# Kernel tuning notes

Measured on AMD Instinct MI355X. Metric: run time of the kernel, lower is better.

## Reference

```python
import jax, jax.numpy as jnp
import numpy as np

N = 10000
E = 320000
IN_DIM = 1
HD = 32
OUT_DIM = 1


def _lin(k, fan_in, fan_out):
    k1, k2 = jax.random.split(k)
    bound = 1.0 / np.sqrt(fan_in)
    W = jax.random.uniform(k1, (fan_in, fan_out), minval=-bound, maxval=bound, dtype=jnp.float32)
    b = jax.random.uniform(k2, (fan_out,), minval=-bound, maxval=bound, dtype=jnp.float32)
    return W, b


def setup_inputs() -> dict:
    key = jax.random.key(0)
    ks = jax.random.split(key, 12)
    sources = jax.random.randint(ks[0], (E,), 0, N)
    dests = jax.random.randint(ks[1], (E,), 0, N)
    weights = jax.random.uniform(ks[2], (E, 1), dtype=jnp.float32)
    x = jax.random.normal(ks[3], (N, IN_DIM), dtype=jnp.float32)
    h = jax.random.normal(ks[4], (N, HD), dtype=jnp.float32)
    W_enc, b_enc = _lin(ks[5], IN_DIM + HD, HD)
    W_msg, b_msg = _lin(ks[6], 2 * HD + 1, HD)
    W_upd, b_upd = _lin(ks[7], 2 * HD, HD)
    W_dec, b_dec = _lin(ks[8], 2 * HD, OUT_DIM)
    W_term, b_term = _lin(ks[9], HD, 1)
    W_pred, b_pred = _lin(ks[10], 2 * HD + 1, 1)
    return {"sources": sources, "dests": dests, "weights": weights, "x": x, "h": h,
            "W_enc": W_enc, "b_enc": b_enc, "W_msg": W_msg, "b_msg": b_msg,
            "W_upd": W_upd, "b_upd": b_upd, "W_dec": W_dec, "b_dec": b_dec,
            "W_term": W_term, "b_term": b_term, "W_pred": W_pred, "b_pred": b_pred}


def reference(sources, dests, weights, x, h, W_enc, b_enc, W_msg, b_msg,
              W_upd, b_upd, W_dec, b_dec, W_term, b_term, W_pred, b_pred):
    n = h.shape[0]
    # Encoder: z = Linear(cat[x, h])
    z = jnp.concatenate([x, h], axis=1) @ W_enc + b_enc  # [N, HD]
    # Processor messages: Linear(cat[z[dest], z[src], w])
    msg_in = jnp.concatenate([z[dests], z[sources], weights], axis=1)  # [E, 2*HD+1]
    messages = msg_in @ W_msg + b_msg  # [E, HD]
    # scatter-amax into destination nodes, -inf (no edge) -> 0
    m = jnp.full((n, HD), -jnp.inf, dtype=z.dtype).at[dests].max(messages)
    m = jnp.where(jnp.isneginf(m), jnp.zeros_like(m), m)
    h_new = jnp.concatenate([z, m], axis=1) @ W_upd + b_upd  # [N, HD]
    # Decoder
    y = jnp.concatenate([z, h_new], axis=1) @ W_dec + b_dec  # [N, 1]
    # Termination: proj of mean node state -> scalar
    t = (h_new.mean(axis=0) @ W_term + b_term).squeeze()
    # Predecessor: dense N x N score matrix, edge entries set to proj score
    pred_in = jnp.concatenate([h_new[dests], h_new[sources], weights], axis=1)
    edge_scores = (pred_in @ W_pred + b_pred)[:, 0]  # [E]
    p = jnp.full((n, n), -1e9, dtype=h_new.dtype).at[dests, sources].set(edge_scores)
    return (y, p, h_new, t)
```

## Files before the change

kernel.cpp:

```cpp
#include <hip/hip_runtime.h>
#include <stdint.h>

namespace {
constexpr int  kN  = 10000;
constexpr int  kE  = 320000;
constexpr long kPOff = 10000;
constexpr long kHOff = 10000L + 100000000L;
constexpr long kTOff = kHOff + 320000L;
constexpr long kP4   = (long)kN * kN / 4;
constexpr long kFillA = kP4 * 15 / 100;
constexpr long kFillB = kP4 * 80 / 100;
constexpr int  kG = 2048;
}

typedef float f32x4 __attribute__((ext_vector_type(4)));

__device__ __forceinline__ float shfl32(float v, int k) { return __shfl(v, k, 32); }

__device__ __forceinline__ void fill_slice(float* __restrict__ p, long lo, long hi)
{
    long idx = (long)blockIdx.x * blockDim.x + threadIdx.x;
    long stride = (long)gridDim.x * blockDim.x;
    f32x4 v = { -1e9f, -1e9f, -1e9f, -1e9f };
    f32x4* p4 = reinterpret_cast<f32x4*>(p);
    for (long i = lo + idx; i < hi; i += stride)
        p4[i] = v;
}

__global__ __launch_bounds__(256) void k1_encz(
    const float* __restrict__ x, const float* __restrict__ h,
    const float* __restrict__ W_enc, const float* __restrict__ b_enc,
    const float* __restrict__ W_msg, const float* __restrict__ b_msg,
    float* __restrict__ z, float* __restrict__ zwd, float* __restrict__ zws,
    float* __restrict__ m, float* __restrict__ sum_h, float* __restrict__ p)
{
    if (blockIdx.x == 0 && threadIdx.x < 32) sum_h[threadIdx.x] = 0.0f;

    int lane = threadIdx.x & 63;
    int wid  = threadIdx.x >> 6;
    int half = lane >> 5;
    int j    = lane & 31;

    for (int i = blockIdx.x * 8 + wid * 2 + half; i < kN; i += kG * 8) {
        float hj = h[(long)i * 32 + j];
        float xi = x[i];
        float zj = fmaf(xi, W_enc[j], b_enc[j]);
#pragma unroll
        for (int k = 0; k < 32; ++k)
            zj = fmaf(shfl32(hj, k), W_enc[(1 + k) * 32 + j], zj);

        z[(long)i * 32 + j] = zj;
        m[(long)i * 32 + j] = -__builtin_inff();

        float dv = b_msg[j], sv = 0.0f;
#pragma unroll
        for (int k = 0; k < 32; ++k) {
            float zk = shfl32(zj, k);
            dv = fmaf(zk, W_msg[k * 32 + j], dv);
            sv = fmaf(zk, W_msg[(32 + k) * 32 + j], sv);
        }
        zwd[(long)i * 32 + j] = dv;
        zws[(long)i * 32 + j] = sv;
    }

    fill_slice(p, 0, kFillA);
}

__global__ __launch_bounds__(256) void k2_msgmax(
    const int* __restrict__ src, const int* __restrict__ dst,
    const float* __restrict__ w, const float* __restrict__ zwd,
    const float* __restrict__ zws, const float* __restrict__ W_msg,
    float* __restrict__ m, float* __restrict__ p)
{
    int lane = threadIdx.x & 63;
    int wid  = threadIdx.x >> 6;
    int half = lane >> 5;
    int j    = lane & 31;
    float Ww = W_msg[64 * 32 + j];
    int gw = blockIdx.x * 4 + wid;
    for (int ep = gw; ep < kE / 2; ep += kG * 4) {
        int e = ep * 2 + half;
        int d = dst[e], s = src[e];
        float val = fmaf(w[e], Ww, zwd[(long)d * 32 + j] + zws[(long)s * 32 + j]);
        float* addr = m + (long)d * 32 + j;
        if (val >= 0.0f)
            atomicMax(reinterpret_cast<int*>(addr), __float_as_int(val));
        else
            atomicMin(reinterpret_cast<unsigned int*>(addr), __float_as_uint(val));
    }

    fill_slice(p, kFillA, kFillB);
}

__global__ __launch_bounds__(256) void k3_updn(
    const float* __restrict__ z, const float* __restrict__ m,
    const float* __restrict__ W_upd, const float* __restrict__ b_upd,
    const float* __restrict__ W_dec, const float* __restrict__ b_dec,
    const float* __restrict__ W_pred,
    float* __restrict__ y_out, float* __restrict__ h_out,
    float* __restrict__ a_out, float* __restrict__ b_out,
    float* __restrict__ sum_h, float* __restrict__ p)
{
    int i = blockIdx.x * 256 + threadIdx.x;
    if (i < ((kN + 255) & ~255)) {
        bool valid = i < kN;
        int ii = valid ? i : (kN - 1);

        float acc[32];
#pragma unroll
        for (int jj = 0; jj < 32; ++jj) acc[jj] = b_upd[jj];
        float yv = b_dec[0];

        const float4* z4 = reinterpret_cast<const float4*>(z + (long)ii * 32);
#pragma unroll
        for (int q = 0; q < 8; ++q) {
            float4 v = z4[q];
            float in0 = v.x, in1 = v.y, in2 = v.z, in3 = v.w;
            int k = q * 4;
            yv = fmaf(in0, W_dec[k + 0], yv);
            yv = fmaf(in1, W_dec[k + 1], yv);
            yv = fmaf(in2, W_dec[k + 2], yv);
            yv = fmaf(in3, W_dec[k + 3], yv);
            const float* W0 = W_upd + (k + 0) * 32;
            const float* W1 = W_upd + (k + 1) * 32;
            const float* W2 = W_upd + (k + 2) * 32;
            const float* W3 = W_upd + (k + 3) * 32;
#pragma unroll
            for (int jj = 0; jj < 32; ++jj) acc[jj] = fmaf(in0, W0[jj], acc[jj]);
#pragma unroll
            for (int jj = 0; jj < 32; ++jj) acc[jj] = fmaf(in1, W1[jj], acc[jj]);
#pragma unroll
            for (int jj = 0; jj < 32; ++jj) acc[jj] = fmaf(in2, W2[jj], acc[jj]);
#pragma unroll
            for (int jj = 0; jj < 32; ++jj) acc[jj] = fmaf(in3, W3[jj], acc[jj]);
        }

        const float NEG_INF = -__builtin_inff();
        const float4* m4 = reinterpret_cast<const float4*>(m + (long)ii * 32);
#pragma unroll
        for (int q = 0; q < 8; ++q) {
            float4 v = m4[q];
            float in0 = (v.x == NEG_INF) ? 0.0f : v.x;
            float in1 = (v.y == NEG_INF) ? 0.0f : v.y;
            float in2 = (v.z == NEG_INF) ? 0.0f : v.z;
            float in3 = (v.w == NEG_INF) ? 0.0f : v.w;
            int k = 32 + q * 4;
            const float* W0 = W_upd + (k + 0) * 32;
            const float* W1 = W_upd + (k + 1) * 32;
            const float* W2 = W_upd + (k + 2) * 32;
            const float* W3 = W_upd + (k + 3) * 32;
#pragma unroll
            for (int jj = 0; jj < 32; ++jj) acc[jj] = fmaf(in0, W0[jj], acc[jj]);
#pragma unroll
            for (int jj = 0; jj < 32; ++jj) acc[jj] = fmaf(in1, W1[jj], acc[jj]);
#pragma unroll
            for (int jj = 0; jj < 32; ++jj) acc[jj] = fmaf(in2, W2[jj], acc[jj]);
#pragma unroll
            for (int jj = 0; jj < 32; ++jj) acc[jj] = fmaf(in3, W3[jj], acc[jj]);
        }

        float av = 0.0f, bv = 0.0f;
#pragma unroll
        for (int k = 0; k < 32; ++k) {
            yv = fmaf(acc[k], W_dec[32 + k], yv);
            av = fmaf(acc[k], W_pred[k], av);
            bv = fmaf(acc[k], W_pred[32 + k], bv);
        }

        if (valid) {
            y_out[i] = yv;
            a_out[i] = av;
            b_out[i] = bv;
            float4* hrow = reinterpret_cast<float4*>(h_out + (long)i * 32);
#pragma unroll
            for (int q = 0; q < 8; ++q)
                hrow[q] = make_float4(acc[q * 4 + 0], acc[q * 4 + 1],
                                      acc[q * 4 + 2], acc[q * 4 + 3]);
        }

#pragma unroll
        for (int jj = 0; jj < 32; ++jj) {
            float v = valid ? acc[jj] : 0.0f;
#pragma unroll
            for (int off = 32; off; off >>= 1) v += __shfl_down(v, off, 64);
            if ((threadIdx.x & 63) == 0) atomicAdd(sum_h + jj, v);
        }
    }

    fill_slice(p, kFillB, kP4);
}

__global__ __launch_bounds__(256) void k4_pred(
    const int* __restrict__ src, const int* __restrict__ dst,
    const float* __restrict__ w, const float* __restrict__ a,
    const float* __restrict__ b, const float* __restrict__ W_pred,
    const float* __restrict__ b_pred, const float* __restrict__ sum_h,
    const float* __restrict__ W_term, const float* __restrict__ b_term,
    float* __restrict__ t_out, float* __restrict__ p)
{
    if (blockIdx.x == 0 && threadIdx.x < 64) {
        int l = threadIdx.x;
        float s = (l < 32) ? (sum_h[l] * (1.0f / (float)kN)) * W_term[l] : 0.0f;
#pragma unroll
        for (int off = 32; off; off >>= 1) s += __shfl_down(s, off, 64);
        if (l == 0) t_out[0] = s + b_term[0];
    }

    for (int e = blockIdx.x * 256 + threadIdx.x; e < kE; e += kG * 256) {
        int d = dst[e], s = src[e];
        float score = a[d] + b[s] + fmaf(w[e], W_pred[64], b_pred[0]);
        p[(long)d * kN + s] = score;
    }
}

extern "C" void kernel_launch(void* const* d_in, const int* in_sizes, int n_in,
                              void* d_out, int out_size, void* d_ws, size_t ws_size,
                              hipStream_t stream)
{
    const int*   sources = (const int*)d_in[0];
    const int*   dests   = (const int*)d_in[1];
    const float* weights = (const float*)d_in[2];
    const float* x       = (const float*)d_in[3];
    const float* h       = (const float*)d_in[4];
    const float* W_enc   = (const float*)d_in[5];
    const float* b_enc   = (const float*)d_in[6];
    const float* W_msg   = (const float*)d_in[7];
    const float* b_msg   = (const float*)d_in[8];
    const float* W_upd   = (const float*)d_in[9];
    const float* b_upd   = (const float*)d_in[10];
    const float* W_dec   = (const float*)d_in[11];
    const float* b_dec   = (const float*)d_in[12];
    const float* W_term  = (const float*)d_in[13];
    const float* b_term  = (const float*)d_in[14];
    const float* W_pred  = (const float*)d_in[15];
    const float* b_pred  = (const float*)d_in[16];

    float* out   = (float*)d_out;
    float* y_out = out;
    float* p_out = out + kPOff;
    float* h_out = out + kHOff;
    float* t_out = out + kTOff;

    float* z     = (float*)d_ws;
    float* m     = z   + (long)kN * 32;
    float* zwd   = m   + (long)kN * 32;
    float* zws   = zwd + (long)kN * 32;
    float* a_ws  = zws + (long)kN * 32;
    float* b_ws  = a_ws + kN;
    float* sum_h = b_ws + kN;

    k1_encz<<<kG, 256, 0, stream>>>(x, h, W_enc, b_enc, W_msg, b_msg,
                                    z, zwd, zws, m, sum_h, p_out);
    k2_msgmax<<<kG, 256, 0, stream>>>(sources, dests, weights, zwd, zws, W_msg,
                                      m, p_out);
    k3_updn<<<kG, 256, 0, stream>>>(z, m, W_upd, b_upd, W_dec, b_dec, W_pred,
                                    y_out, h_out, a_ws, b_ws, sum_h, p_out);
    k4_pred<<<kG, 256, 0, stream>>>(sources, dests, weights, a_ws, b_ws,
                                    W_pred, b_pred, sum_h, W_term, b_term,
                                    t_out, p_out);
}
```

Measured before the change: 599.1 us.

## Replicate max-aggregation buffer and move dense fill into a standalone kernel

The scatter-max target is replicated eight ways, with each block choosing a replica by block index. This spreads atomic contention, and the update kernel then reduces the replicas with fmax. The 400MB fill of the predecessor matrix is no longer split across the first three kernels; it now runs in its own kernel just before the edge-scatter kernel, and grid sizes are matched to each kernel's work. The cost is eight times more memory to initialise and to read back in the update step. Moving the fill out of the other kernels also removes any overlap it had with their compute.

```diff
diff --git a/kernel.cpp b/kernel.cpp
--- a/kernel.cpp
+++ b/kernel.cpp
@@ -4,193 +4,201 @@
 namespace {
 constexpr int  kN  = 10000;
 constexpr int  kE  = 320000;
+constexpr int  kR  = 8;
 constexpr long kPOff = 10000;
 constexpr long kHOff = 10000L + 100000000L;
 constexpr long kTOff = kHOff + 320000L;
-constexpr long kP4   = (long)kN * kN / 4;
-constexpr long kFillA = kP4 * 15 / 100;
-constexpr long kFillB = kP4 * 80 / 100;
-constexpr int  kG = 2048;
 }
 
 typedef float f32x4 __attribute__((ext_vector_type(4)));
 
 __device__ __forceinline__ float shfl32(float v, int k) { return __shfl(v, k, 32); }
-
-__device__ __forceinline__ void fill_slice(float* __restrict__ p, long lo, long hi)
-{
-    long idx = (long)blockIdx.x * blockDim.x + threadIdx.x;
-    long stride = (long)gridDim.x * blockDim.x;
-    f32x4 v = { -1e9f, -1e9f, -1e9f, -1e9f };
-    f32x4* p4 = reinterpret_cast<f32x4*>(p);
-    for (long i = lo + idx; i < hi; i += stride)
-        p4[i] = v;
-}
 
 __global__ __launch_bounds__(256) void k1_encz(
     const float* __restrict__ x, const float* __restrict__ h,
     const float* __restrict__ W_enc, const float* __restrict__ b_enc,
     const float* __restrict__ W_msg, const float* __restrict__ b_msg,
     float* __restrict__ z, float* __restrict__ zwd, float* __restrict__ zws,
-    float* __restrict__ m, float* __restrict__ sum_h, float* __restrict__ p)
+    float* __restrict__ m_rep, float* __restrict__ sum_h)
 {
     if (blockIdx.x == 0 && threadIdx.x < 32) sum_h[threadIdx.x] = 0.0f;
+
+    {
+        const float NEG_INF = -__builtin_inff();
+        f32x4 vinf = { NEG_INF, NEG_INF, NEG_INF, NEG_INF };
+        f32x4* r4 = reinterpret_cast<f32x4*>(m_rep);
+        long total4 = (long)kR * kN * 32 / 4;
+        long idx = (long)blockIdx.x * 256 + threadIdx.x;
+        long stride = (long)gridDim.x * 256;
+        for (long i = idx; i < total4; i += stride) r4[i] = vinf;
+    }
 
     int lane = threadIdx.x & 63;
     int wid  = threadIdx.x >> 6;
     int half = lane >> 5;
     int j    = lane & 31;
-
-    for (int i = blockIdx.x * 8 + wid * 2 + half; i < kN; i += kG * 8) {
-        float hj = h[(long)i * 32 + j];
-        float xi = x[i];
-        float zj = fmaf(xi, W_enc[j], b_enc[j]);
-#pragma unroll
-        for (int k = 0; k < 32; ++k)
-            zj = fmaf(shfl32(hj, k), W_enc[(1 + k) * 32 + j], zj);
-
-        z[(long)i * 32 + j] = zj;
-        m[(long)i * 32 + j] = -__builtin_inff();
-
-        float dv = b_msg[j], sv = 0.0f;
-#pragma unroll
-        for (int k = 0; k < 32; ++k) {
-            float zk = shfl32(zj, k);
-            dv = fmaf(zk, W_msg[k * 32 + j], dv);
-            sv = fmaf(zk, W_msg[(32 + k) * 32 + j], sv);
-        }
-        zwd[(long)i * 32 + j] = dv;
-        zws[(long)i * 32 + j] = sv;
-    }
-
-    fill_slice(p, 0, kFillA);
+    int i = blockIdx.x * 8 + wid * 2 + half;
+    if (i >= kN) return;
+
+    float hj = h[(long)i * 32 + j];
+    float xi = x[i];
+    float zj = fmaf(xi, W_enc[j], b_enc[j]);
+#pragma unroll
+    for (int k = 0; k < 32; ++k)
+        zj = fmaf(shfl32(hj, k), W_enc[(1 + k) * 32 + j], zj);
+
+    z[(long)i * 32 + j] = zj;
+
+    float dv = b_msg[j], sv = 0.0f;
+#pragma unroll
+    for (int k = 0; k < 32; ++k) {
+        float zk = shfl32(zj, k);
+        dv = fmaf(zk, W_msg[k * 32 + j], dv);
+        sv = fmaf(zk, W_msg[(32 + k) * 32 + j], sv);
+    }
+    zwd[(long)i * 32 + j] = dv;
+    zws[(long)i * 32 + j] = sv;
 }
 
 __global__ __launch_bounds__(256) void k2_msgmax(
     const int* __restrict__ src, const int* __restrict__ dst,
     const float* __restrict__ w, const float* __restrict__ zwd,
     const float* __restrict__ zws, const float* __restrict__ W_msg,
-    float* __restrict__ m, float* __restrict__ p)
+    float* __restrict__ m_rep)
 {
     int lane = threadIdx.x & 63;
     int wid  = threadIdx.x >> 6;
     int half = lane >> 5;
     int j    = lane & 31;
     float Ww = W_msg[64 * 32 + j];
+    float* mr = m_rep + (long)(blockIdx.x & (kR - 1)) * kN * 32;
+
     int gw = blockIdx.x * 4 + wid;
-    for (int ep = gw; ep < kE / 2; ep += kG * 4) {
+    int nw = gridDim.x * 4;
+    for (int ep = gw; ep < kE / 2; ep += nw) {
         int e = ep * 2 + half;
         int d = dst[e], s = src[e];
         float val = fmaf(w[e], Ww, zwd[(long)d * 32 + j] + zws[(long)s * 32 + j]);
-        float* addr = m + (long)d * 32 + j;
+        float* addr = mr + (long)d * 32 + j;
         if (val >= 0.0f)
             atomicMax(reinterpret_cast<int*>(addr), __float_as_int(val));
         else
             atomicMin(reinterpret_cast<unsigned int*>(addr), __float_as_uint(val));
     }
-
-    fill_slice(p, kFillA, kFillB);
 }
 
 __global__ __launch_bounds__(256) void k3_updn(
-    const float* __restrict__ z, const float* __restrict__ m,
+    const float* __restrict__ z, const float* __restrict__ m_rep,
     const float* __restrict__ W_upd, const float* __restrict__ b_upd,
     const float* __restrict__ W_dec, const float* __restrict__ b_dec,
     const float* __restrict__ W_pred,
     float* __restrict__ y_out, float* __restrict__ h_out,
     float* __restrict__ a_out, float* __restrict__ b_out,
-    float* __restrict__ sum_h, float* __restrict__ p)
+    float* __restrict__ sum_h)
 {
     int i = blockIdx.x * 256 + threadIdx.x;
-    if (i < ((kN + 255) & ~255)) {
-        bool valid = i < kN;
-        int ii = valid ? i : (kN - 1);
-
-        float acc[32];
-#pragma unroll
-        for (int jj = 0; jj < 32; ++jj) acc[jj] = b_upd[jj];
-        float yv = b_dec[0];
-
-        const float4* z4 = reinterpret_cast<const float4*>(z + (long)ii * 32);
-#pragma unroll
-        for (int q = 0; q < 8; ++q) {
-            float4 v = z4[q];
-            float in0 = v.x, in1 = v.y, in2 = v.z, in3 = v.w;
-            int k = q * 4;
-            yv = fmaf(in0, W_dec[k + 0], yv);
-            yv = fmaf(in1, W_dec[k + 1], yv);
-            yv = fmaf(in2, W_dec[k + 2], yv);
-            yv = fmaf(in3, W_dec[k + 3], yv);
-            const float* W0 = W_upd + (k + 0) * 32;
-            const float* W1 = W_upd + (k + 1) * 32;
-            const float* W2 = W_upd + (k + 2) * 32;
-            const float* W3 = W_upd + (k + 3) * 32;
-#pragma unroll
-            for (int jj = 0; jj < 32; ++jj) acc[jj] = fmaf(in0, W0[jj], acc[jj]);
-#pragma unroll
-            for (int jj = 0; jj < 32; ++jj) acc[jj] = fmaf(in1, W1[jj], acc[jj]);
-#pragma unroll
-            for (int jj = 0; jj < 32; ++jj) acc[jj] = fmaf(in2, W2[jj], acc[jj]);
-#pragma unroll
-            for (int jj = 0; jj < 32; ++jj) acc[jj] = fmaf(in3, W3[jj], acc[jj]);
+    bool valid = i < kN;
+    int ii = valid ? i : (kN - 1);
+
+    float acc[32];
+#pragma unroll
+    for (int jj = 0; jj < 32; ++jj) acc[jj] = b_upd[jj];
+    float yv = b_dec[0];
+
+    const float4* z4 = reinterpret_cast<const float4*>(z + (long)ii * 32);
+#pragma unroll
+    for (int q = 0; q < 8; ++q) {
+        float4 v = z4[q];
+        float in0 = v.x, in1 = v.y, in2 = v.z, in3 = v.w;
+        int k = q * 4;
+        yv = fmaf(in0, W_dec[k + 0], yv);
+        yv = fmaf(in1, W_dec[k + 1], yv);
+        yv = fmaf(in2, W_dec[k + 2], yv);
+        yv = fmaf(in3, W_dec[k + 3], yv);
+        const float* W0 = W_upd + (k + 0) * 32;
+        const float* W1 = W_upd + (k + 1) * 32;
+        const float* W2 = W_upd + (k + 2) * 32;
+        const float* W3 = W_upd + (k + 3) * 32;
+#pragma unroll
+        for (int jj = 0; jj < 32; ++jj) acc[jj] = fmaf(in0, W0[jj], acc[jj]);
+#pragma unroll
+        for (int jj = 0; jj < 32; ++jj) acc[jj] = fmaf(in1, W1[jj], acc[jj]);
+#pragma unroll
+        for (int jj = 0; jj < 32; ++jj) acc[jj] = fmaf(in2, W2[jj], acc[jj]);
+#pragma unroll
+        for (int jj = 0; jj < 32; ++jj) acc[jj] = fmaf(in3, W3[jj], acc[jj]);
+    }
+
+    const float NEG_INF = -__builtin_inff();
+#pragma unroll
+    for (int q = 0; q < 8; ++q) {
+        const float4* m4 = reinterpret_cast<const float4*>(m_rep + (long)ii * 32) + q;
+        float4 v = *m4;
+#pragma unroll
+        for (int r = 1; r < kR; ++r) {
+            float4 t = *(m4 + (long)r * kN * 8);
+            v.x = fmaxf(v.x, t.x); v.y = fmaxf(v.y, t.y);
+            v.z = fmaxf(v.z, t.z); v.w = fmaxf(v.w, t.w);
         }
-
-        const float NEG_INF = -__builtin_inff();
-        const float4* m4 = reinterpret_cast<const float4*>(m + (long)ii * 32);
-#pragma unroll
-        for (int q = 0; q < 8; ++q) {
-            float4 v = m4[q];
-            float in0 = (v.x == NEG_INF) ? 0.0f : v.x;
-            float in1 = (v.y == NEG_INF) ? 0.0f : v.y;
-            float in2 = (v.z == NEG_INF) ? 0.0f : v.z;
-            float in3 = (v.w == NEG_INF) ? 0.0f : v.w;
-            int k = 32 + q * 4;
-            const float* W0 = W_upd + (k + 0) * 32;
-            const float* W1 = W_upd + (k + 1) * 32;
-            const float* W2 = W_upd + (k + 2) * 32;
-            const float* W3 = W_upd + (k + 3) * 32;
-#pragma unroll
-            for (int jj = 0; jj < 32; ++jj) acc[jj] = fmaf(in0, W0[jj], acc[jj]);
-#pragma unroll
-            for (int jj = 0; jj < 32; ++jj) acc[jj] = fmaf(in1, W1[jj], acc[jj]);
-#pragma unroll
-            for (int jj = 0; jj < 32; ++jj) acc[jj] = fmaf(in2, W2[jj], acc[jj]);
-#pragma unroll
-            for (int jj = 0; jj < 32; ++jj) acc[jj] = fmaf(in3, W3[jj], acc[jj]);
-        }
-
-        float av = 0.0f, bv = 0.0f;
-#pragma unroll
-        for (int k = 0; k < 32; ++k) {
-            yv = fmaf(acc[k], W_dec[32 + k], yv);
-            av = fmaf(acc[k], W_pred[k], av);
-            bv = fmaf(acc[k], W_pred[32 + k], bv);
-        }
-
-        if (valid) {
-            y_out[i] = yv;
-            a_out[i] = av;
-            b_out[i] = bv;
-            float4* hrow = reinterpret_cast<float4*>(h_out + (long)i * 32);
-#pragma unroll
-            for (int q = 0; q < 8; ++q)
-                hrow[q] = make_float4(acc[q * 4 + 0], acc[q * 4 + 1],
-                                      acc[q * 4 + 2], acc[q * 4 + 3]);
-        }
-
-#pragma unroll
-        for (int jj = 0; jj < 32; ++jj) {
-            float v = valid ? acc[jj] : 0.0f;
-#pragma unroll
-            for (int off = 32; off; off >>= 1) v += __shfl_down(v, off, 64);
-            if ((threadIdx.x & 63) == 0) atomicAdd(sum_h + jj, v);
-        }
-    }
-
-    fill_slice(p, kFillB, kP4);
-}
-
-__global__ __launch_bounds__(256) void k4_pred(
+        float in0 = (v.x == NEG_INF) ? 0.0f : v.x;
+        float in1 = (v.y == NEG_INF) ? 0.0f : v.y;
+        float in2 = (v.z == NEG_INF) ? 0.0f : v.z;
+        float in3 = (v.w == NEG_INF) ? 0.0f : v.w;
+        int k = 32 + q * 4;
+        const float* W0 = W_upd + (k + 0) * 32;
+        const float* W1 = W_upd + (k + 1) * 32;
+        const float* W2 = W_upd + (k + 2) * 32;
+        const float* W3 = W_upd + (k + 3) * 32;
+#pragma unroll
+        for (int jj = 0; jj < 32; ++jj) acc[jj] = fmaf(in0, W0[jj], acc[jj]);
+#pragma unroll
+        for (int jj = 0; jj < 32; ++jj) acc[jj] = fmaf(in1, W1[jj], acc[jj]);
+#pragma unroll
+        for (int jj = 0; jj < 32; ++jj) acc[jj] = fmaf(in2, W2[jj], acc[jj]);
+#pragma unroll
+        for (int jj = 0; jj < 32; ++jj) acc[jj] = fmaf(in3, W3[jj], acc[jj]);
+    }
+
+    float av = 0.0f, bv = 0.0f;
+#pragma unroll
+    for (int k = 0; k < 32; ++k) {
+        yv = fmaf(acc[k], W_dec[32 + k], yv);
+        av = fmaf(acc[k], W_pred[k], av);
+        bv = fmaf(acc[k], W_pred[32 + k], bv);
+    }
+
+    if (valid) {
+        y_out[i] = yv;
+        a_out[i] = av;
+        b_out[i] = bv;
+        float4* hrow = reinterpret_cast<float4*>(h_out + (long)i * 32);
+#pragma unroll
+        for (int q = 0; q < 8; ++q)
+            hrow[q] = make_float4(acc[q * 4 + 0], acc[q * 4 + 1],
+                                  acc[q * 4 + 2], acc[q * 4 + 3]);
+    }
+
+#pragma unroll
+    for (int jj = 0; jj < 32; ++jj) {
+        float v = valid ? acc[jj] : 0.0f;
+#pragma unroll
+        for (int off = 32; off; off >>= 1) v += __shfl_down(v, off, 64);
+        if ((threadIdx.x & 63) == 0) atomicAdd(sum_h + jj, v);
+    }
+}
+
+__global__ __launch_bounds__(256) void k4_fill(float* __restrict__ p)
+{
+    long idx = (long)blockIdx.x * 256 + threadIdx.x;
+    long stride = (long)gridDim.x * 256;
+    const long total4 = (long)kN * (long)kN / 4;
+    f32x4 v = { -1e9f, -1e9f, -1e9f, -1e9f };
+    f32x4* p4 = reinterpret_cast<f32x4*>(p);
+    for (long i = idx; i < total4; i += stride)
+        p4[i] = v;
+}
+
+__global__ __launch_bounds__(256) void k5_pred(
     const int* __restrict__ src, const int* __restrict__ dst,
     const float* __restrict__ w, const float* __restrict__ a,
     const float* __restrict__ b, const float* __restrict__ W_pred,
@@ -206,11 +214,11 @@
         if (l == 0) t_out[0] = s + b_term[0];
     }
 
-    for (int e = blockIdx.x * 256 + threadIdx.x; e < kE; e += kG * 256) {
-        int d = dst[e], s = src[e];
-        float score = a[d] + b[s] + fmaf(w[e], W_pred[64], b_pred[0]);
-        p[(long)d * kN + s] = score;
-    }
+    int e = blockIdx.x * 256 + threadIdx.x;
+    if (e >= kE) return;
+    int d = dst[e], s = src[e];
+    float score = a[d] + b[s] + fmaf(w[e], W_pred[64], b_pred[0]);
+    p[(long)d * kN + s] = score;
 }
 
 extern "C" void kernel_launch(void* const* d_in, const int* in_sizes, int n_in,
@@ -242,20 +250,20 @@
     float* t_out = out + kTOff;
 
     float* z     = (float*)d_ws;
-    float* m     = z   + (long)kN * 32;
-    float* zwd   = m   + (long)kN * 32;
+    float* zwd   = z   + (long)kN * 32;
     float* zws   = zwd + (long)kN * 32;
     float* a_ws  = zws + (long)kN * 32;
     float* b_ws  = a_ws + kN;
     float* sum_h = b_ws + kN;
-
-    k1_encz<<<kG, 256, 0, stream>>>(x, h, W_enc, b_enc, W_msg, b_msg,
-                                    z, zwd, zws, m, sum_h, p_out);
-    k2_msgmax<<<kG, 256, 0, stream>>>(sources, dests, weights, zwd, zws, W_msg,
-                                      m, p_out);
-    k3_updn<<<kG, 256, 0, stream>>>(z, m, W_upd, b_upd, W_dec, b_dec, W_pred,
-                                    y_out, h_out, a_ws, b_ws, sum_h, p_out);
-    k4_pred<<<kG, 256, 0, stream>>>(sources, dests, weights, a_ws, b_ws,
-                                    W_pred, b_pred, sum_h, W_term, b_term,
-                                    t_out, p_out);
-}
+    float* m_rep = sum_h + 32;
+
+    k1_encz<<<(kN + 7) / 8, 256, 0, stream>>>(x, h, W_enc, b_enc, W_msg, b_msg,
+                                              z, zwd, zws, m_rep, sum_h);
+    k2_msgmax<<<2048, 256, 0, stream>>>(sources, dests, weights, zwd, zws, W_msg, m_rep);
+    k3_updn<<<(kN + 255) / 256, 256, 0, stream>>>(z, m_rep, W_upd, b_upd, W_dec, b_dec,
+                                                  W_pred, y_out, h_out, a_ws, b_ws, sum_h);
+    k4_fill<<<8192, 256, 0, stream>>>(p_out);
+    k5_pred<<<(kE + 255) / 256, 256, 0, stream>>>(sources, dests, weights, a_ws, b_ws,
+                                                  W_pred, b_pred, sum_h, W_term, b_term,
+                                                  t_out, p_out);
+}
```

Result: no change. 609.1 us (+1.7%).

## Consolidate dense P fill into message kernel via block specialization

Applied to the files above, without the earlier changes.

Moves the entire -1e9 fill of the N×N score matrix into the edge message/scatter-max kernel, dedicating odd blocks to the fill and even blocks to the atomic scatter. The encoder, update and predecessor kernels lose their fill slices and are launched with exact-size grids instead of grid-stride loops over 2048 blocks. The aim is to overlap the bandwidth-bound fill with the latency-bound atomic scatter and to make the other kernels short. In exchange, only half the blocks of one kernel drive the 400 MB fill, which may underuse memory bandwidth compared with spreading it across three kernels.

```diff
diff --git a/kernel.cpp b/kernel.cpp
--- a/kernel.cpp
+++ b/kernel.cpp
@@ -8,31 +8,18 @@
 constexpr long kHOff = 10000L + 100000000L;
 constexpr long kTOff = kHOff + 320000L;
 constexpr long kP4   = (long)kN * kN / 4;
-constexpr long kFillA = kP4 * 15 / 100;
-constexpr long kFillB = kP4 * 80 / 100;
-constexpr int  kG = 2048;
 }
 
 typedef float f32x4 __attribute__((ext_vector_type(4)));
 
 __device__ __forceinline__ float shfl32(float v, int k) { return __shfl(v, k, 32); }
-
-__device__ __forceinline__ void fill_slice(float* __restrict__ p, long lo, long hi)
-{
-    long idx = (long)blockIdx.x * blockDim.x + threadIdx.x;
-    long stride = (long)gridDim.x * blockDim.x;
-    f32x4 v = { -1e9f, -1e9f, -1e9f, -1e9f };
-    f32x4* p4 = reinterpret_cast<f32x4*>(p);
-    for (long i = lo + idx; i < hi; i += stride)
-        p4[i] = v;
-}
 
 __global__ __launch_bounds__(256) void k1_encz(
     const float* __restrict__ x, const float* __restrict__ h,
     const float* __restrict__ W_enc, const float* __restrict__ b_enc,
     const float* __restrict__ W_msg, const float* __restrict__ b_msg,
     float* __restrict__ z, float* __restrict__ zwd, float* __restrict__ zws,
-    float* __restrict__ m, float* __restrict__ sum_h, float* __restrict__ p)
+    float* __restrict__ m, float* __restrict__ sum_h)
 {
     if (blockIdx.x == 0 && threadIdx.x < 32) sum_h[threadIdx.x] = 0.0f;
 
@@ -40,56 +27,64 @@
     int wid  = threadIdx.x >> 6;
     int half = lane >> 5;
     int j    = lane & 31;
-
-    for (int i = blockIdx.x * 8 + wid * 2 + half; i < kN; i += kG * 8) {
-        float hj = h[(long)i * 32 + j];
-        float xi = x[i];
-        float zj = fmaf(xi, W_enc[j], b_enc[j]);
-#pragma unroll
-        for (int k = 0; k < 32; ++k)
-            zj = fmaf(shfl32(hj, k), W_enc[(1 + k) * 32 + j], zj);
-
-        z[(long)i * 32 + j] = zj;
-        m[(long)i * 32 + j] = -__builtin_inff();
-
-        float dv = b_msg[j], sv = 0.0f;
-#pragma unroll
-        for (int k = 0; k < 32; ++k) {
-            float zk = shfl32(zj, k);
-            dv = fmaf(zk, W_msg[k * 32 + j], dv);
-            sv = fmaf(zk, W_msg[(32 + k) * 32 + j], sv);
-        }
-        zwd[(long)i * 32 + j] = dv;
-        zws[(long)i * 32 + j] = sv;
-    }
-
-    fill_slice(p, 0, kFillA);
-}
-
-__global__ __launch_bounds__(256) void k2_msgmax(
+    int i = blockIdx.x * 8 + wid * 2 + half;
+    if (i >= kN) return;
+
+    float hj = h[(long)i * 32 + j];
+    float xi = x[i];
+    float zj = fmaf(xi, W_enc[j], b_enc[j]);
+#pragma unroll
+    for (int k = 0; k < 32; ++k)
+        zj = fmaf(shfl32(hj, k), W_enc[(1 + k) * 32 + j], zj);
+
+    z[(long)i * 32 + j] = zj;
+    m[(long)i * 32 + j] = -__builtin_inff();
+
+    float dv = b_msg[j], sv = 0.0f;
+#pragma unroll
+    for (int k = 0; k < 32; ++k) {
+        float zk = shfl32(zj, k);
+        dv = fmaf(zk, W_msg[k * 32 + j], dv);
+        sv = fmaf(zk, W_msg[(32 + k) * 32 + j], sv);
+    }
+    zwd[(long)i * 32 + j] = dv;
+    zws[(long)i * 32 + j] = sv;
+}
+
+__global__ __launch_bounds__(256) void k2_work(
     const int* __restrict__ src, const int* __restrict__ dst,
     const float* __restrict__ w, const float* __restrict__ zwd,
     const float* __restrict__ zws, const float* __restrict__ W_msg,
     float* __restrict__ m, float* __restrict__ p)
 {
-    int lane = threadIdx.x & 63;
-    int wid  = threadIdx.x >> 6;
-    int half = lane >> 5;
-    int j    = lane & 31;
-    float Ww = W_msg[64 * 32 + j];
-    int gw = blockIdx.x * 4 + wid;
-    for (int ep = gw; ep < kE / 2; ep += kG * 4) {
-        int e = ep * 2 + half;
-        int d = dst[e], s = src[e];
-        float val = fmaf(w[e], Ww, zwd[(long)d * 32 + j] + zws[(long)s * 32 + j]);
-        float* addr = m + (long)d * 32 + j;
-        if (val >= 0.0f)
-            atomicMax(reinterpret_cast<int*>(addr), __float_as_int(val));
-        else
-            atomicMin(reinterpret_cast<unsigned int*>(addr), __float_as_uint(val));
-    }
-
-    fill_slice(p, kFillA, kFillB);
+    if (blockIdx.x & 1) {
+        long fb = blockIdx.x >> 1;
+        long idx = fb * 256 + threadIdx.x;
+        long stride = 1024L * 256;
+        f32x4 v = { -1e9f, -1e9f, -1e9f, -1e9f };
+        f32x4* p4 = reinterpret_cast<f32x4*>(p);
+        for (long i = idx; i < kP4; i += stride)
+            p4[i] = v;
+    } else {
+        int lane = threadIdx.x & 63;
+        int wid  = threadIdx.x >> 6;
+        int half = lane >> 5;
+        int j    = lane & 31;
+        float Ww = W_msg[64 * 32 + j];
+        int mb = blockIdx.x >> 1;
+        int gw = mb * 4 + wid;
+        int nw = 1024 * 4;
+        for (int ep = gw; ep < kE / 2; ep += nw) {
+            int e = ep * 2 + half;
+            int d = dst[e], s = src[e];
+            float val = fmaf(w[e], Ww, zwd[(long)d * 32 + j] + zws[(long)s * 32 + j]);
+            float* addr = m + (long)d * 32 + j;
+            if (val >= 0.0f)
+                atomicMax(reinterpret_cast<int*>(addr), __float_as_int(val));
+            else
+                atomicMin(reinterpret_cast<unsigned int*>(addr), __float_as_uint(val));
+        }
+    }
 }
 
 __global__ __launch_bounds__(256) void k3_updn(
@@ -99,95 +94,91 @@
     const float* __restrict__ W_pred,
     float* __restrict__ y_out, float* __restrict__ h_out,
     float* __restrict__ a_out, float* __restrict__ b_out,
-    float* __restrict__ sum_h, float* __restrict__ p)
+    float* __restrict__ sum_h)
 {
     int i = blockIdx.x * 256 + threadIdx.x;
-    if (i < ((kN + 255) & ~255)) {
-        bool valid = i < kN;
-        int ii = valid ? i : (kN - 1);
-
-        float acc[32];
-#pragma unroll
-        for (int jj = 0; jj < 32; ++jj) acc[jj] = b_upd[jj];
-        float yv = b_dec[0];
-
-        const float4* z4 = reinterpret_cast<const float4*>(z + (long)ii * 32);
-#pragma unroll
-        for (int q = 0; q < 8; ++q) {
-            float4 v = z4[q];
-            float in0 = v.x, in1 = v.y, in2 = v.z, in3 = v.w;
-            int k = q * 4;
-            yv = fmaf(in0, W_dec[k + 0], yv);
-            yv = fmaf(in1, W_dec[k + 1], yv);
-            yv = fmaf(in2, W_dec[k + 2], yv);
-            yv = fmaf(in3, W_dec[k + 3], yv);
-            const float* W0 = W_upd + (k + 0) * 32;
-            const float* W1 = W_upd + (k + 1) * 32;
-            const float* W2 = W_upd + (k + 2) * 32;
-            const float* W3 = W_upd + (k + 3) * 32;
-#pragma unroll
-            for (int jj = 0; jj < 32; ++jj) acc[jj] = fmaf(in0, W0[jj], acc[jj]);
-#pragma unroll
-            for (int jj = 0; jj < 32; ++jj) acc[jj] = fmaf(in1, W1[jj], acc[jj]);
-#pragma unroll
-            for (int jj = 0; jj < 32; ++jj) acc[jj] = fmaf(in2, W2[jj], acc[jj]);
-#pragma unroll
-            for (int jj = 0; jj < 32; ++jj) acc[jj] = fmaf(in3, W3[jj], acc[jj]);
-        }
-
-        const float NEG_INF = -__builtin_inff();
-        const float4* m4 = reinterpret_cast<const float4*>(m + (long)ii * 32);
-#pragma unroll
-        for (int q = 0; q < 8; ++q) {
-            float4 v = m4[q];
-            float in0 = (v.x == NEG_INF) ? 0.0f : v.x;
-            float in1 = (v.y == NEG_INF) ? 0.0f : v.y;
-            float in2 = (v.z == NEG_INF) ? 0.0f : v.z;
-            float in3 = (v.w == NEG_INF) ? 0.0f : v.w;
-            int k = 32 + q * 4;
-            const float* W0 = W_upd + (k + 0) * 32;
-            const float* W1 = W_upd + (k + 1) * 32;
-            const float* W2 = W_upd + (k + 2) * 32;
-            const float* W3 = W_upd + (k + 3) * 32;
-#pragma unroll
-            for (int jj = 0; jj < 32; ++jj) acc[jj] = fmaf(in0, W0[jj], acc[jj]);
-#pragma unroll
-            for (int jj = 0; jj < 32; ++jj) acc[jj] = fmaf(in1, W1[jj], acc[jj]);
-#pragma unroll
-            for (int jj = 0; jj < 32; ++jj) acc[jj] = fmaf(in2, W2[jj], acc[jj]);
-#pragma unroll
-            for (int jj = 0; jj < 32; ++jj) acc[jj] = fmaf(in3, W3[jj], acc[jj]);
-        }
-
-        float av = 0.0f, bv = 0.0f;
-#pragma unroll
-        for (int k = 0; k < 32; ++k) {
-            yv = fmaf(acc[k], W_dec[32 + k], yv);
-            av = fmaf(acc[k], W_pred[k], av);
-            bv = fmaf(acc[k], W_pred[32 + k], bv);
-        }
-
-        if (valid) {
-            y_out[i] = yv;
-            a_out[i] = av;
-            b_out[i] = bv;
-            float4* hrow = reinterpret_cast<float4*>(h_out + (long)i * 32);
-#pragma unroll
-            for (int q = 0; q < 8; ++q)
-                hrow[q] = make_float4(acc[q * 4 + 0], acc[q * 4 + 1],
-                                      acc[q * 4 + 2], acc[q * 4 + 3]);
-        }
-
-#pragma unroll
-        for (int jj = 0; jj < 32; ++jj) {
-            float v = valid ? acc[jj] : 0.0f;
-#pragma unroll
-            for (int off = 32; off; off >>= 1) v += __shfl_down(v, off, 64);
-            if ((threadIdx.x & 63) == 0) atomicAdd(sum_h + jj, v);
-        }
-    }
-
-    fill_slice(p, kFillB, kP4);
+    bool valid = i < kN;
+    int ii = valid ? i : (kN - 1);
+
+    float acc[32];
+#pragma unroll
+    for (int jj = 0; jj < 32; ++jj) acc[jj] = b_upd[jj];
+    float yv = b_dec[0];
+
+    const float4* z4 = reinterpret_cast<const float4*>(z + (long)ii * 32);
+#pragma unroll
+    for (int q = 0; q < 8; ++q) {
+        float4 v = z4[q];
+        float in0 = v.x, in1 = v.y, in2 = v.z, in3 = v.w;
+        int k = q * 4;
+        yv = fmaf(in0, W_dec[k + 0], yv);
+        yv = fmaf(in1, W_dec[k + 1], yv);
+        yv = fmaf(in2, W_dec[k + 2], yv);
+        yv = fmaf(in3, W_dec[k + 3], yv);
+        const float* W0 = W_upd + (k + 0) * 32;
+        const float* W1 = W_upd + (k + 1) * 32;
+        const float* W2 = W_upd + (k + 2) * 32;
+        const float* W3 = W_upd + (k + 3) * 32;
+#pragma unroll
+        for (int jj = 0; jj < 32; ++jj) acc[jj] = fmaf(in0, W0[jj], acc[jj]);
+#pragma unroll
+        for (int jj = 0; jj < 32; ++jj) acc[jj] = fmaf(in1, W1[jj], acc[jj]);
+#pragma unroll
+        for (int jj = 0; jj < 32; ++jj) acc[jj] = fmaf(in2, W2[jj], acc[jj]);
+#pragma unroll
+        for (int jj = 0; jj < 32; ++jj) acc[jj] = fmaf(in3, W3[jj], acc[jj]);
+    }
+
+    const float NEG_INF = -__builtin_inff();
+    const float4* m4 = reinterpret_cast<const float4*>(m + (long)ii * 32);
+#pragma unroll
+    for (int q = 0; q < 8; ++q) {
+        float4 v = m4[q];
+        float in0 = (v.x == NEG_INF) ? 0.0f : v.x;
+        float in1 = (v.y == NEG_INF) ? 0.0f : v.y;
+        float in2 = (v.z == NEG_INF) ? 0.0f : v.z;
+        float in3 = (v.w == NEG_INF) ? 0.0f : v.w;
+        int k = 32 + q * 4;
+        const float* W0 = W_upd + (k + 0) * 32;
+        const float* W1 = W_upd + (k + 1) * 32;
+        const float* W2 = W_upd + (k + 2) * 32;
+        const float* W3 = W_upd + (k + 3) * 32;
+#pragma unroll
+        for (int jj = 0; jj < 32; ++jj) acc[jj] = fmaf(in0, W0[jj], acc[jj]);
+#pragma unroll
+        for (int jj = 0; jj < 32; ++jj) acc[jj] = fmaf(in1, W1[jj], acc[jj]);
+#pragma unroll
+        for (int jj = 0; jj < 32; ++jj) acc[jj] = fmaf(in2, W2[jj], acc[jj]);
+#pragma unroll
+        for (int jj = 0; jj < 32; ++jj) acc[jj] = fmaf(in3, W3[jj], acc[jj]);
+    }
+
+    float av = 0.0f, bv = 0.0f;
+#pragma unroll
+    for (int k = 0; k < 32; ++k) {
+        yv = fmaf(acc[k], W_dec[32 + k], yv);
+        av = fmaf(acc[k], W_pred[k], av);
+        bv = fmaf(acc[k], W_pred[32 + k], bv);
+    }
+
+    if (valid) {
+        y_out[i] = yv;
+        a_out[i] = av;
+        b_out[i] = bv;
+        float4* hrow = reinterpret_cast<float4*>(h_out + (long)i * 32);
+#pragma unroll
+        for (int q = 0; q < 8; ++q)
+            hrow[q] = make_float4(acc[q * 4 + 0], acc[q * 4 + 1],
+                                  acc[q * 4 + 2], acc[q * 4 + 3]);
+    }
+
+#pragma unroll
+    for (int jj = 0; jj < 32; ++jj) {
+        float v = valid ? acc[jj] : 0.0f;
+#pragma unroll
+        for (int off = 32; off; off >>= 1) v += __shfl_down(v, off, 64);
+        if ((threadIdx.x & 63) == 0) atomicAdd(sum_h + jj, v);
+    }
 }
 
 __global__ __launch_bounds__(256) void k4_pred(
@@ -206,11 +197,11 @@
         if (l == 0) t_out[0] = s + b_term[0];
     }
 
-    for (int e = blockIdx.x * 256 + threadIdx.x; e < kE; e += kG * 256) {
-        int d = dst[e], s = src[e];
-        float score = a[d] + b[s] + fmaf(w[e], W_pred[64], b_pred[0]);
-        p[(long)d * kN + s] = score;
-    }
+    int e = blockIdx.x * 256 + threadIdx.x;
+    if (e >= kE) return;
+    int d = dst[e], s = src[e];
+    float score = a[d] + b[s] + fmaf(w[e], W_pred[64], b_pred[0]);
+    p[(long)d * kN + s] = score;
 }
 
 extern "C" void kernel_launch(void* const* d_in, const int* in_sizes, int n_in,
@@ -249,13 +240,13 @@
     float* b_ws  = a_ws + kN;
     float* sum_h = b_ws + kN;
 
-    k1_encz<<<kG, 256, 0, stream>>>(x, h, W_enc, b_enc, W_msg, b_msg,
-                                    z, zwd, zws, m, sum_h, p_out);
-    k2_msgmax<<<kG, 256, 0, stream>>>(sources, dests, weights, zwd, zws, W_msg,
+    k1_encz<<<(kN + 7) / 8, 256, 0, stream>>>(x, h, W_enc, b_enc, W_msg, b_msg,
+                                              z, zwd, zws, m, sum_h);
+    k2_work<<<2048, 256, 0, stream>>>(sources, dests, weights, zwd, zws, W_msg,
                                       m, p_out);
-    k3_updn<<<kG, 256, 0, stream>>>(z, m, W_upd, b_upd, W_dec, b_dec, W_pred,
-                                    y_out, h_out, a_ws, b_ws, sum_h, p_out);
-    k4_pred<<<kG, 256, 0, stream>>>(sources, dests, weights, a_ws, b_ws,
-                                    W_pred, b_pred, sum_h, W_term, b_term,
-                                    t_out, p_out);
-}
+    k3_updn<<<(kN + 255) / 256, 256, 0, stream>>>(z, m, W_upd, b_upd, W_dec, b_dec,
+                                                  W_pred, y_out, h_out, a_ws, b_ws, sum_h);
+    k4_pred<<<(kE + 255) / 256, 256, 0, stream>>>(sources, dests, weights, a_ws, b_ws,
+                                                  W_pred, b_pred, sum_h, W_term, b_term,
+                                                  t_out, p_out);
+}
```

Measured after the change: 590.8 us. No clear change (-1.4%).
